# Kernel optimization log

Hardware: AMD Instinct MI355X
Metric: run time of the kernel (lower is better)

The kernel has to match this reference:

```python
import jax, jax.numpy as jnp
import numpy as np

N = 100_000        # nodes
F_IN = 1024        # input features
H1, C1 = 8, 8      # layer-1 heads, per-head channels (concat -> 64)
C_OUT = 40         # num classes (layer-2, heads=1, concat=False)
E = 3_200_000      # directed edges (avg degree 32)
NEG_SLOPE = 0.2    # PyG GATConv default leaky_relu slope


def setup_inputs() -> dict:
    key = jax.random.key(0)
    ks = jax.random.split(key, 10)
    x = jax.random.normal(ks[0], (N, F_IN), jnp.float32)
    edge_index = jax.random.randint(ks[1], (2, E), 0, N, dtype=jnp.int32)
    s1 = 1.0 / np.sqrt(F_IN)
    W1 = jax.random.normal(ks[2], (F_IN, H1 * C1), jnp.float32) * s1
    sa = 1.0 / np.sqrt(C1)
    att_src1 = jax.random.normal(ks[3], (H1, C1), jnp.float32) * sa
    att_dst1 = jax.random.normal(ks[4], (H1, C1), jnp.float32) * sa
    b1 = jnp.zeros((H1 * C1,), jnp.float32)
    s2 = 1.0 / np.sqrt(H1 * C1)
    W2 = jax.random.normal(ks[5], (H1 * C1, C_OUT), jnp.float32) * s2
    so = 1.0 / np.sqrt(C_OUT)
    att_src2 = jax.random.normal(ks[6], (1, C_OUT), jnp.float32) * so
    att_dst2 = jax.random.normal(ks[7], (1, C_OUT), jnp.float32) * so
    b2 = jnp.zeros((C_OUT,), jnp.float32)
    return {"x": x, "edge_index": edge_index, "W1": W1, "att_src1": att_src1,
            "att_dst1": att_dst1, "b1": b1, "W2": W2, "att_src2": att_src2,
            "att_dst2": att_dst2, "b2": b2}


def gat_layer(x, src, dst, W, a_src, a_dst, b, heads, ch, concat, n):
    # per-head linear projection: [n, heads, ch]
    xw = (x @ W).reshape(n, heads, ch)
    # per-node attention logits: [n, heads]
    al_src = jnp.einsum('nhc,hc->nh', xw, a_src)
    al_dst = jnp.einsum('nhc,hc->nh', xw, a_dst)
    # per-edge scores (message src -> dst): [e, heads]
    e = jax.nn.leaky_relu(al_src[src] + al_dst[dst], NEG_SLOPE)
    # segment softmax over incoming edges of each dst node
    m = jax.ops.segment_max(e, dst, num_segments=n)          # [n, heads]
    p = jnp.exp(e - m[dst])
    denom = jax.ops.segment_sum(p, dst, num_segments=n)      # [n, heads]
    alpha = p / (denom[dst] + 1e-16)                          # [e, heads]
    # weighted scatter-sum of source features
    out = jax.ops.segment_sum(xw[src] * alpha[:, :, None], dst, num_segments=n)
    out = out.reshape(n, heads * ch) if concat else out.mean(axis=1)
    return out + b


def reference(x, edge_index, W1, att_src1, att_dst1, b1, W2, att_src2, att_dst2, b2):
    n = x.shape[0]
    # PyG GATConv default: add self loops
    loop = jnp.arange(n, dtype=edge_index.dtype)
    src = jnp.concatenate([edge_index[0], loop])
    dst = jnp.concatenate([edge_index[1], loop])
    h = jax.nn.elu(gat_layer(x, src, dst, W1, att_src1, att_dst1, b1, H1, C1, True, n))
    h = gat_layer(h, src, dst, W2, att_src2, att_dst2, b2, 1, C_OUT, False, n)
    return jax.nn.log_softmax(h, axis=1)
```

## Files before the change

### kernel.cpp

```cpp
#include <hip/hip_runtime.h>
#include <hip/hip_bf16.h>
#include <cstdint>
#include <cstddef>

#define F_IN 1024
#define F1 64
#define H1 8
#define C1 8
#define C_OUT 40
#define XW2S 64
#define NEG 0.2f
#define LOG2E 1.442695040888963387f
#define B1 256
#define BSHIFT 8
#define BNODES 256

typedef __attribute__((ext_vector_type(8))) short short8;
typedef __attribute__((ext_vector_type(4))) float f32x4;

static __device__ __forceinline__ unsigned short f2bf(float f) {
  union { float f; unsigned u; } v; v.f = f;
  unsigned r = v.u + 0x7fff + ((v.u >> 16) & 1);
  return (unsigned short)(r >> 16);
}
static __device__ __forceinline__ float bf2f(unsigned short h) {
  union { unsigned u; float f; } v; v.u = ((unsigned)h) << 16; return v.f;
}
static __device__ __forceinline__ unsigned pkbf(float a, float b) {
  union { __hip_bfloat162 h; unsigned u; } c;
  c.h = __float22bfloat162_rn(float2{a, b});
  return c.u;
}
static __device__ __forceinline__ int rfl(int v) {
  return __builtin_amdgcn_readfirstlane(v);
}

__global__ __launch_bounds__(256) void w1cvt_kernel(const float* __restrict__ W1,
                                                    unsigned short* __restrict__ w1t) {
  int i = blockIdx.x * 256 + threadIdx.x;
  int c = i >> 10, k = i & 1023;
  w1t[i] = f2bf(W1[(size_t)k * F1 + c]);
}

__global__ __launch_bounds__(256) void k1_hist_gemm(const float* __restrict__ x,
    const unsigned short* __restrict__ w1t, unsigned short* __restrict__ xw1,
    const int* __restrict__ dst, int* __restrict__ cnt, int n, int e, int nbuck) {
  const int bid = blockIdx.x;
  const int tid = threadIdx.x;
  if (bid < B1) {
    __shared__ int lh[512];
    lh[tid] = 0; lh[tid + 256] = 0;
    __syncthreads();
    int chunk = (e + B1 - 1) / B1;
    int s = bid * chunk, en = min(e, s + chunk);
    for (int i = s + tid; i < en; i += 256) atomicAdd(&lh[dst[i] >> BSHIFT], 1);
    __syncthreads();
    for (int b = tid; b < nbuck; b += 256) cnt[b * B1 + bid] = lh[b];
    return;
  }
  const int gb = bid - B1;
  const int wv = tid >> 6;
  const int l = tid & 63;
  const int lr = l & 15;
  const int lg = l >> 4;
  const int rowBase = gb * 128 + wv * 32;
  int r0 = rowBase + lr, r1 = rowBase + 16 + lr;
  int r0c = r0 < n ? r0 : (n - 1);
  int r1c = r1 < n ? r1 : (n - 1);
  const float* px0 = x + (size_t)r0c * F_IN + lg * 8;
  const float* px1 = x + (size_t)r1c * F_IN + lg * 8;

  f32x4 acc00 = {0.f,0.f,0.f,0.f}, acc01 = acc00, acc02 = acc00, acc03 = acc00;
  f32x4 acc10 = acc00, acc11 = acc00, acc12 = acc00, acc13 = acc00;

#pragma unroll 2
  for (int k0 = 0; k0 < F_IN; k0 += 32) {
    float4 xa0 = *(const float4*)(px0 + k0);
    float4 xb0 = *(const float4*)(px0 + k0 + 4);
    float4 xa1 = *(const float4*)(px1 + k0);
    float4 xb1 = *(const float4*)(px1 + k0 + 4);
    union { short8 s; unsigned u[4]; } a0, a1;
    a0.u[0] = pkbf(xa0.x, xa0.y); a0.u[1] = pkbf(xa0.z, xa0.w);
    a0.u[2] = pkbf(xb0.x, xb0.y); a0.u[3] = pkbf(xb0.z, xb0.w);
    a1.u[0] = pkbf(xa1.x, xa1.y); a1.u[1] = pkbf(xa1.z, xa1.w);
    a1.u[2] = pkbf(xb1.x, xb1.y); a1.u[3] = pkbf(xb1.z, xb1.w);
    const size_t kOff = (size_t)(k0 + lg * 8);
    short8 b0 = *(const short8*)(w1t + (size_t)(0 * 16 + lr) * F_IN + kOff);
    short8 b1 = *(const short8*)(w1t + (size_t)(1 * 16 + lr) * F_IN + kOff);
    short8 b2 = *(const short8*)(w1t + (size_t)(2 * 16 + lr) * F_IN + kOff);
    short8 b3 = *(const short8*)(w1t + (size_t)(3 * 16 + lr) * F_IN + kOff);
    acc00 = __builtin_amdgcn_mfma_f32_16x16x32_bf16(a0.s, b0, acc00, 0, 0, 0);
    acc01 = __builtin_amdgcn_mfma_f32_16x16x32_bf16(a0.s, b1, acc01, 0, 0, 0);
    acc02 = __builtin_amdgcn_mfma_f32_16x16x32_bf16(a0.s, b2, acc02, 0, 0, 0);
    acc03 = __builtin_amdgcn_mfma_f32_16x16x32_bf16(a0.s, b3, acc03, 0, 0, 0);
    acc10 = __builtin_amdgcn_mfma_f32_16x16x32_bf16(a1.s, b0, acc10, 0, 0, 0);
    acc11 = __builtin_amdgcn_mfma_f32_16x16x32_bf16(a1.s, b1, acc11, 0, 0, 0);
    acc12 = __builtin_amdgcn_mfma_f32_16x16x32_bf16(a1.s, b2, acc12, 0, 0, 0);
    acc13 = __builtin_amdgcn_mfma_f32_16x16x32_bf16(a1.s, b3, acc13, 0, 0, 0);
  }

#pragma unroll
  for (int r = 0; r < 4; ++r) {
    int o0 = rowBase + lg * 4 + r;
    if (o0 < n) {
      unsigned short* po = xw1 + (size_t)o0 * F1 + lr;
      po[0]  = f2bf(acc00[r]);
      po[16] = f2bf(acc01[r]);
      po[32] = f2bf(acc02[r]);
      po[48] = f2bf(acc03[r]);
    }
    int o1 = rowBase + 16 + lg * 4 + r;
    if (o1 < n) {
      unsigned short* po = xw1 + (size_t)o1 * F1 + lr;
      po[0]  = f2bf(acc10[r]);
      po[16] = f2bf(acc11[r]);
      po[32] = f2bf(acc12[r]);
      po[48] = f2bf(acc13[r]);
    }
  }
}

__global__ __launch_bounds__(256) void al1_kernel(const unsigned short* __restrict__ xw1,
    const float* __restrict__ asrc, const float* __restrict__ adst,
    float* __restrict__ al_src, float* __restrict__ al_dst, int n) {
  int id = blockIdx.x * 256 + threadIdx.x;
  if (id >= n * H1) return;
  int node = id >> 3, h = id & 7;
  union { short8 s; unsigned short u[8]; } rowv;
  rowv.s = *(const short8*)(xw1 + (size_t)node * F1 + h * C1);
  float s = 0.f, d = 0.f;
#pragma unroll
  for (int c = 0; c < C1; ++c) {
    float v = bf2f(rowv.u[c]);
    s += v * asrc[h * C1 + c];
    d += v * adst[h * C1 + c];
  }
  al_src[id] = s * LOG2E;
  al_dst[id] = d * LOG2E;
}

__global__ __launch_bounds__(256) void scan1_kernel(const int* __restrict__ in,
    int* __restrict__ excl, int* __restrict__ bsum, int len) {
  __shared__ int s[256];
  int tid = threadIdx.x;
  int gid = blockIdx.x * 256 + tid;
  int v = gid < len ? in[gid] : 0;
  s[tid] = v;
  __syncthreads();
  for (int ofs = 1; ofs < 256; ofs <<= 1) {
    int t = (tid >= ofs) ? s[tid - ofs] : 0;
    __syncthreads();
    s[tid] += t;
    __syncthreads();
  }
  if (gid < len) excl[gid] = s[tid] - v;
  if (tid == 255) bsum[blockIdx.x] = s[255];
}

__global__ __launch_bounds__(1024) void scan2_kernel(int* __restrict__ bsum, int nb) {
  __shared__ int s[1024];
  int tid = threadIdx.x;
  int v = tid < nb ? bsum[tid] : 0;
  s[tid] = v;
  __syncthreads();
  for (int ofs = 1; ofs < 1024; ofs <<= 1) {
    int t = (tid >= ofs) ? s[tid - ofs] : 0;
    __syncthreads();
    s[tid] += t;
    __syncthreads();
  }
  if (tid < nb) bsum[tid] = s[tid] - v;
}

__global__ __launch_bounds__(256) void binscatter_kernel(const int* __restrict__ src,
    const int* __restrict__ dst, const int* __restrict__ cntS,
    const int* __restrict__ bsum, unsigned* __restrict__ binned, int e, int nbuck) {
  __shared__ int lcur[512];
  int tid = threadIdx.x, blk = blockIdx.x;
  for (int b = tid; b < nbuck; b += 256) lcur[b] = cntS[b * B1 + blk] + bsum[b];
  __syncthreads();
  int chunk = (e + gridDim.x - 1) / gridDim.x;
  int s = blk * chunk, en = min(e, s + chunk);
  for (int i = s + tid; i < en; i += 256) {
    int d = dst[i];
    int pos = atomicAdd(&lcur[d >> BSHIFT], 1);
    binned[pos] = ((unsigned)(d & (BNODES - 1)) << 23) | (unsigned)src[i];
  }
}

__global__ __launch_bounds__(256) void bucket_csr_kernel(const unsigned* __restrict__ binned,
    const int* __restrict__ bsum, int* __restrict__ deg, int* __restrict__ off,
    int* __restrict__ csr, int e, int n, int nbuck) {
  int q = blockIdx.x, tid = threadIdx.x;
  int eBase = bsum[q];
  int eEnd = (q + 1 < nbuck) ? bsum[q + 1] : e;
  __shared__ int nh[BNODES], sc[BNODES], cu[BNODES];
  nh[tid] = 0;
  __syncthreads();
  for (int i = eBase + tid; i < eEnd; i += 256) atomicAdd(&nh[binned[i] >> 23], 1);
  __syncthreads();
  int v = nh[tid];
  sc[tid] = v;
  __syncthreads();
  for (int ofs = 1; ofs < BNODES; ofs <<= 1) {
    int t = (tid >= ofs) ? sc[tid - ofs] : 0;
    __syncthreads();
    sc[tid] += t;
    __syncthreads();
  }
  int ex = sc[tid] - v;
  cu[tid] = ex;
  int node0 = q * BNODES + tid;
  if (node0 < n) { deg[node0] = v; off[node0] = eBase + ex; }
  __syncthreads();
  for (int i = eBase + tid; i < eEnd; i += 256) {
    unsigned w = binned[i];
    int pos = eBase + atomicAdd(&cu[w >> 23], 1);
    csr[pos] = (int)(w & 0x7FFFFF);
  }
}

__global__ __launch_bounds__(256) void gat1_agg(const unsigned short* __restrict__ xw1,
    const float* __restrict__ al_src, const float* __restrict__ al_dst,
    const int* __restrict__ csr, const int* __restrict__ off, const int* __restrict__ deg,
    const float* __restrict__ b1, float* __restrict__ h1, int n) {
  const int node = rfl((int)((blockIdx.x * blockDim.x + threadIdx.x) >> 6));
  if (node >= n) return;
  const int lane = threadIdx.x & 63;
  const int half = lane >> 5;
  const int c2 = lane & 31;
  const int h = c2 >> 2;
  const int base = rfl(off[node]);
  const int cnt = rfl(deg[node]);
  const float adst = al_dst[node * H1 + h];
  const int* __restrict__ csrp = csr + base;
  const char* xwB = (const char*)xw1;
  const char* alB = (const char*)al_src;
  const int cOff = c2 << 2;
  const int hOff = h << 2;

  float acc0 = 0.f, acc1 = 0.f, l = 0.f;

#define PAIR_BODY(wv_, av_) { \
    float t = (av_) + adst; \
    float sc = fmaxf(t, NEG * t); \
    float p = __builtin_amdgcn_exp2f(sc); \
    acc0 = fmaf(p, bf2f((unsigned short)((wv_) & 0xffffu)), acc0); \
    acc1 = fmaf(p, bf2f((unsigned short)((wv_) >> 16)), acc1); \
    l += p; }

  int it = 0;
  for (; it + 16 <= cnt; it += 16) {
    int xo[8];
#pragma unroll
    for (int jp = 0; jp < 8; ++jp) {
      int s0 = rfl(csrp[it + 2 * jp]) << 7;
      int s1 = rfl(csrp[it + 2 * jp + 1]) << 7;
      xo[jp] = half ? s1 : s0;
    }
    unsigned wv[8]; float av[8];
#pragma unroll
    for (int jp = 0; jp < 8; ++jp) {
      wv[jp] = *(const unsigned*)(xwB + xo[jp] + cOff);
      av[jp] = *(const float*)(alB + (xo[jp] >> 2) + hOff);
    }
#pragma unroll
    for (int jp = 0; jp < 8; ++jp) PAIR_BODY(wv[jp], av[jp]);
  }
  for (; it + 2 <= cnt; it += 2) {
    int s0 = rfl(csrp[it]) << 7;
    int s1 = rfl(csrp[it + 1]) << 7;
    int bs = half ? s1 : s0;
    unsigned w = *(const unsigned*)(xwB + bs + cOff);
    float av = *(const float*)(alB + (bs >> 2) + hOff);
    PAIR_BODY(w, av);
  }
  {
    const bool odd = (it < cnt);
    int sA = odd ? rfl(csrp[it]) : node;
    int bs = (half ? node : sA) << 7;
    unsigned w = *(const unsigned*)(xwB + bs + cOff);
    float av = *(const float*)(alB + (bs >> 2) + hOff);
    float t = av + adst;
    float sc = fmaxf(t, NEG * t);
    float p = __builtin_amdgcn_exp2f(sc);
    if (!odd && half) p = 0.f;
    acc0 = fmaf(p, bf2f((unsigned short)(w & 0xffffu)), acc0);
    acc1 = fmaf(p, bf2f((unsigned short)(w >> 16)), acc1);
    l += p;
  }
#undef PAIR_BODY

  acc0 += __shfl_xor(acc0, 32);
  acc1 += __shfl_xor(acc1, 32);
  l    += __shfl_xor(l, 32);
  if (half == 0) {
    float inv = 1.f / (l + 1e-16f);
    float2 bv = *(const float2*)(b1 + (c2 << 1));
    float o0 = acc0 * inv + bv.x;
    float o1 = acc1 * inv + bv.y;
    o0 = o0 > 0.f ? o0 : __expf(o0) - 1.f;
    o1 = o1 > 0.f ? o1 : __expf(o1) - 1.f;
    *(float2*)(h1 + (size_t)node * F1 + (c2 << 1)) = make_float2(o0, o1);
  }
}

__global__ __launch_bounds__(256) void gemm2_kernel(const float* __restrict__ h1,
    const float* __restrict__ W2, const float* __restrict__ asrc,
    const float* __restrict__ adst, unsigned short* __restrict__ xw2,
    float* __restrict__ alS2, float* __restrict__ alD2, int n) {
  __shared__ float ws[F1 * C_OUT];
  __shared__ float wsa[C_OUT], wsd[C_OUT];
  int tid = threadIdx.x;
  for (int i = tid; i < F1 * C_OUT; i += 256) ws[i] = W2[i];
  if (tid < C_OUT) { wsa[tid] = asrc[tid]; wsd[tid] = adst[tid]; }
  __syncthreads();
  int node = blockIdx.x * 256 + tid;
  if (node >= n) return;
  const float4* row4 = (const float4*)(h1 + (size_t)node * F1);
  float acc[C_OUT];
#pragma unroll
  for (int j = 0; j < C_OUT; ++j) acc[j] = 0.f;
#pragma unroll 2
  for (int k4 = 0; k4 < 16; ++k4) {
    float4 xv = row4[k4];
    const float* w0 = &ws[(4 * k4 + 0) * C_OUT];
    const float* w1 = &ws[(4 * k4 + 1) * C_OUT];
    const float* w2 = &ws[(4 * k4 + 2) * C_OUT];
    const float* w3 = &ws[(4 * k4 + 3) * C_OUT];
#pragma unroll
    for (int j = 0; j < C_OUT; j += 4) {
      float4 v0 = *(const float4*)(w0 + j);
      float4 v1 = *(const float4*)(w1 + j);
      float4 v2 = *(const float4*)(w2 + j);
      float4 v3 = *(const float4*)(w3 + j);
      acc[j + 0] += xv.x * v0.x + xv.y * v1.x + xv.z * v2.x + xv.w * v3.x;
      acc[j + 1] += xv.x * v0.y + xv.y * v1.y + xv.z * v2.y + xv.w * v3.y;
      acc[j + 2] += xv.x * v0.z + xv.y * v1.z + xv.z * v2.z + xv.w * v3.z;
      acc[j + 3] += xv.x * v0.w + xv.y * v1.w + xv.z * v2.w + xv.w * v3.w;
    }
  }
  float s = 0.f, d = 0.f;
#pragma unroll
  for (int j = 0; j < C_OUT; ++j) { s += acc[j] * wsa[j]; d += acc[j] * wsd[j]; }
  alS2[node] = s * LOG2E;
  alD2[node] = d * LOG2E;
  unsigned short* orow = xw2 + (size_t)node * XW2S;
#pragma unroll
  for (int j = 0; j < C_OUT; j += 4) {
    ushort4 o;
    o.x = f2bf(acc[j + 0]); o.y = f2bf(acc[j + 1]);
    o.z = f2bf(acc[j + 2]); o.w = f2bf(acc[j + 3]);
    *(ushort4*)(orow + j) = o;
  }
}

__global__ __launch_bounds__(256) void gat2_agg(const unsigned short* __restrict__ xw2,
    const float* __restrict__ alS, const float* __restrict__ alD,
    const int* __restrict__ csr, const int* __restrict__ off, const int* __restrict__ deg,
    const float* __restrict__ b2, float* __restrict__ out, int n) {
  const int node = rfl((int)((blockIdx.x * blockDim.x + threadIdx.x) >> 6));
  if (node >= n) return;
  const int lane = threadIdx.x & 63;
  const int half = lane >> 5;
  const int c2 = lane & 31;
  const bool act = c2 < 20;
  const int c2r = act ? c2 : 0;
  const int base = rfl(off[node]);
  const int cnt = rfl(deg[node]);
  const float adst = alD[node];
  const int* __restrict__ csrp = csr + base;
  const char* xwB = (const char*)xw2;
  const char* alB = (const char*)alS;
  const int cOff = c2r << 2;

  float acc0 = 0.f, acc1 = 0.f, l = 0.f;

#define PAIR_BODY2(wv_, av_) { \
    float t = (av_) + adst; \
    float sc = fmaxf(t, NEG * t); \
    float p = __builtin_amdgcn_exp2f(sc); \
    acc0 = fmaf(p, bf2f((unsigned short)((wv_) & 0xffffu)), acc0); \
    acc1 = fmaf(p, bf2f((unsigned short)((wv_) >> 16)), acc1); \
    l += p; }

  int it = 0;
  for (; it + 16 <= cnt; it += 16) {
    int xo[8];
#pragma unroll
    for (int jp = 0; jp < 8; ++jp) {
      int s0 = rfl(csrp[it + 2 * jp]) << 7;
      int s1 = rfl(csrp[it + 2 * jp + 1]) << 7;
      xo[jp] = half ? s1 : s0;
    }
    unsigned wv[8]; float av[8];
#pragma unroll
    for (int jp = 0; jp < 8; ++jp) {
      wv[jp] = *(const unsigned*)(xwB + xo[jp] + cOff);
      av[jp] = *(const float*)(alB + (xo[jp] >> 5));
    }
#pragma unroll
    for (int jp = 0; jp < 8; ++jp) PAIR_BODY2(wv[jp], av[jp]);
  }
  for (; it + 2 <= cnt; it += 2) {
    int s0 = rfl(csrp[it]) << 7;
    int s1 = rfl(csrp[it + 1]) << 7;
    int bs = half ? s1 : s0;
    unsigned w = *(const unsigned*)(xwB + bs + cOff);
    float av = *(const float*)(alB + (bs >> 5));
    PAIR_BODY2(w, av);
  }
  {
    const bool odd = (it < cnt);
    int sA = odd ? rfl(csrp[it]) : node;
    int bs = (half ? node : sA) << 7;
    unsigned w = *(const unsigned*)(xwB + bs + cOff);
    float av = *(const float*)(alB + (bs >> 5));
    float t = av + adst;
    float sc = fmaxf(t, NEG * t);
    float p = __builtin_amdgcn_exp2f(sc);
    if (!odd && half) p = 0.f;
    acc0 = fmaf(p, bf2f((unsigned short)(w & 0xffffu)), acc0);
    acc1 = fmaf(p, bf2f((unsigned short)(w >> 16)), acc1);
    l += p;
  }
#undef PAIR_BODY2

  acc0 += __shfl_xor(acc0, 32);
  acc1 += __shfl_xor(acc1, 32);
  l    += __shfl_xor(l, 32);

  float inv = 1.f / (l + 1e-16f);
  float v0 = -1e30f, v1 = -1e30f;
  if (act) {
    float2 bv = *(const float2*)(b2 + (c2 << 1));
    v0 = acc0 * inv + bv.x;
    v1 = acc1 * inv + bv.y;
  }
  float mx = fmaxf(v0, v1);
#pragma unroll
  for (int mask = 1; mask <= 16; mask <<= 1) mx = fmaxf(mx, __shfl_xor(mx, mask));
  float e0 = act ? __expf(v0 - mx) : 0.f;
  float e1 = act ? __expf(v1 - mx) : 0.f;
  float sum = e0 + e1;
#pragma unroll
  for (int mask = 1; mask <= 16; mask <<= 1) sum += __shfl_xor(sum, mask);
  if (half == 0 && act) {
    float ls = __logf(sum);
    *(float2*)(out + (size_t)node * C_OUT + (c2 << 1)) =
        make_float2(v0 - mx - ls, v1 - mx - ls);
  }
}

extern "C" void kernel_launch(void* const* d_in, const int* in_sizes, int n_in,
                              void* d_out, int out_size, void* d_ws, size_t ws_size,
                              hipStream_t stream) {
  const float* x   = (const float*)d_in[0];
  const int*   ei  = (const int*)d_in[1];
  const float* W1  = (const float*)d_in[2];
  const float* as1 = (const float*)d_in[3];
  const float* ad1 = (const float*)d_in[4];
  const float* b1  = (const float*)d_in[5];
  const float* W2  = (const float*)d_in[6];
  const float* as2 = (const float*)d_in[7];
  const float* ad2 = (const float*)d_in[8];
  const float* b2  = (const float*)d_in[9];
  float* out = (float*)d_out;

  const int n = in_sizes[0] / F_IN;
  const int e = in_sizes[1] / 2;
  const int* srcIdx = ei;
  const int* dstIdx = ei + e;
  const int nbuck = (n + BNODES - 1) >> BSHIFT;
  const int clen = nbuck * B1;

  char* p = (char*)d_ws;
  auto take = [&](size_t bytes) {
    char* q = p;
    p += (bytes + 255) & ~(size_t)255;
    return q;
  };
  unsigned short* xw1 = (unsigned short*)take((size_t)n * F1 * 2);
  float* h1           = (float*)take((size_t)n * F1 * 4);
  unsigned short* xw2 = (unsigned short*)take((size_t)n * XW2S * 2);
  unsigned short* w1t = (unsigned short*)take((size_t)F_IN * F1 * 2);
  float* alS1 = (float*)take((size_t)n * H1 * 4);
  float* alD1 = (float*)take((size_t)n * H1 * 4);
  float* alS2 = (float*)take((size_t)n * 4);
  float* alD2 = (float*)take((size_t)n * 4);
  int* deg  = (int*)take((size_t)n * 4);
  int* offb = (int*)take((size_t)n * 4);
  int* cnt  = (int*)take((size_t)clen * 4);
  int* cntS = (int*)take((size_t)clen * 4);
  int* bsum = (int*)take(4096);
  unsigned* binned = (unsigned*)take((size_t)e * 4);
  int* csr  = (int*)take((size_t)e * 4);

  dim3 b256(256);
  const int gB = (n + 127) / 128;
  w1cvt_kernel<<<dim3((F_IN * F1) / 256), b256, 0, stream>>>(W1, w1t);
  k1_hist_gemm<<<dim3(B1 + gB), b256, 0, stream>>>(x, w1t, xw1, dstIdx, cnt, n, e, nbuck);
  al1_kernel<<<dim3((n * H1 + 255) / 256), b256, 0, stream>>>(xw1, as1, ad1, alS1, alD1, n);

  int nbScan = (clen + 255) / 256;
  scan1_kernel<<<dim3(nbScan), b256, 0, stream>>>(cnt, cntS, bsum, clen);
  scan2_kernel<<<dim3(1), dim3(1024), 0, stream>>>(bsum, nbScan);
  binscatter_kernel<<<dim3(B1), b256, 0, stream>>>(srcIdx, dstIdx, cntS, bsum, binned, e, nbuck);
  bucket_csr_kernel<<<dim3(nbuck), b256, 0, stream>>>(binned, bsum, deg, offb, csr, e, n, nbuck);

  gat1_agg<<<dim3((n + 3) / 4), b256, 0, stream>>>(xw1, alS1, alD1, csr, offb, deg, b1, h1, n);
  gemm2_kernel<<<dim3((n + 255) / 256), b256, 0, stream>>>(h1, W2, as2, ad2, xw2, alS2, alD2, n);
  gat2_agg<<<dim3((n + 3) / 4), b256, 0, stream>>>(xw2, alS2, alD2, csr, offb, deg, b2, out, n);
}
```

Before: 408.7 us.

## Regroup preprocessing kernels to overlap graph binning with dense GEMM work

Reorders the launch sequence so the histogram is fused with W1 conversion, the bin-scatter is fused with the layer-1 GEMM, and the bucket CSR build is fused with the attention-logit kernel. Blocks of different roles in one launch run concurrently, so memory-bound scatter work overlaps the compute-bound GEMM. It also cuts the number of launches. The risk is that heterogeneous blocks compete for occupancy, and the GEMM now waits for the scans to finish.

Result: slower. 433.4 us (+6.0%).

```diff
diff --git a/kernel.cpp b/kernel.cpp
--- a/kernel.cpp
+++ b/kernel.cpp
@@ -35,16 +35,9 @@
   return __builtin_amdgcn_readfirstlane(v);
 }
 
-__global__ __launch_bounds__(256) void w1cvt_kernel(const float* __restrict__ W1,
-                                                    unsigned short* __restrict__ w1t) {
-  int i = blockIdx.x * 256 + threadIdx.x;
-  int c = i >> 10, k = i & 1023;
-  w1t[i] = f2bf(W1[(size_t)k * F1 + c]);
-}
-
-__global__ __launch_bounds__(256) void k1_hist_gemm(const float* __restrict__ x,
-    const unsigned short* __restrict__ w1t, unsigned short* __restrict__ xw1,
-    const int* __restrict__ dst, int* __restrict__ cnt, int n, int e, int nbuck) {
+__global__ __launch_bounds__(256) void k0_hist_w1cvt(const int* __restrict__ dst,
+    int* __restrict__ cnt, const float* __restrict__ W1,
+    unsigned short* __restrict__ w1t, int e, int nbuck) {
   const int bid = blockIdx.x;
   const int tid = threadIdx.x;
   if (bid < B1) {
@@ -56,6 +49,64 @@
     for (int i = s + tid; i < en; i += 256) atomicAdd(&lh[dst[i] >> BSHIFT], 1);
     __syncthreads();
     for (int b = tid; b < nbuck; b += 256) cnt[b * B1 + bid] = lh[b];
+    return;
+  }
+  int i = (bid - B1) * 256 + tid;
+  int c = i >> 10, k = i & 1023;
+  w1t[i] = f2bf(W1[(size_t)k * F1 + c]);
+}
+
+__global__ __launch_bounds__(256) void scan1_kernel(const int* __restrict__ in,
+    int* __restrict__ excl, int* __restrict__ bsum, int len) {
+  __shared__ int s[256];
+  int tid = threadIdx.x;
+  int gid = blockIdx.x * 256 + tid;
+  int v = gid < len ? in[gid] : 0;
+  s[tid] = v;
+  __syncthreads();
+  for (int ofs = 1; ofs < 256; ofs <<= 1) {
+    int t = (tid >= ofs) ? s[tid - ofs] : 0;
+    __syncthreads();
+    s[tid] += t;
+    __syncthreads();
+  }
+  if (gid < len) excl[gid] = s[tid] - v;
+  if (tid == 255) bsum[blockIdx.x] = s[255];
+}
+
+__global__ __launch_bounds__(1024) void scan2_kernel(int* __restrict__ bsum, int nb) {
+  __shared__ int s[1024];
+  int tid = threadIdx.x;
+  int v = tid < nb ? bsum[tid] : 0;
+  s[tid] = v;
+  __syncthreads();
+  for (int ofs = 1; ofs < 1024; ofs <<= 1) {
+    int t = (tid >= ofs) ? s[tid - ofs] : 0;
+    __syncthreads();
+    s[tid] += t;
+    __syncthreads();
+  }
+  if (tid < nb) bsum[tid] = s[tid] - v;
+}
+
+__global__ __launch_bounds__(256) void k3_scatter_gemm(const float* __restrict__ x,
+    const unsigned short* __restrict__ w1t, unsigned short* __restrict__ xw1,
+    const int* __restrict__ src, const int* __restrict__ dst,
+    const int* __restrict__ cntS, const int* __restrict__ bsum,
+    unsigned* __restrict__ binned, int n, int e, int nbuck) {
+  const int bid = blockIdx.x;
+  const int tid = threadIdx.x;
+  if (bid < B1) {
+    __shared__ int lcur[512];
+    for (int b = tid; b < nbuck; b += 256) lcur[b] = cntS[b * B1 + bid] + bsum[b];
+    __syncthreads();
+    int chunk = (e + B1 - 1) / B1;
+    int s = bid * chunk, en = min(e, s + chunk);
+    for (int i = s + tid; i < en; i += 256) {
+      int d = dst[i];
+      int pos = atomicAdd(&lcur[d >> BSHIFT], 1);
+      binned[pos] = ((unsigned)(d & (BNODES - 1)) << 23) | (unsigned)src[i];
+    }
     return;
   }
   const int gb = bid - B1;
@@ -120,10 +171,44 @@
   }
 }
 
-__global__ __launch_bounds__(256) void al1_kernel(const unsigned short* __restrict__ xw1,
+__global__ __launch_bounds__(256) void k4_bucket_al1(const unsigned* __restrict__ binned,
+    const int* __restrict__ bsum, int* __restrict__ deg, int* __restrict__ off,
+    int* __restrict__ csr, const unsigned short* __restrict__ xw1,
     const float* __restrict__ asrc, const float* __restrict__ adst,
-    float* __restrict__ al_src, float* __restrict__ al_dst, int n) {
-  int id = blockIdx.x * 256 + threadIdx.x;
+    float* __restrict__ al_src, float* __restrict__ al_dst, int e, int n, int nbuck) {
+  const int bid = blockIdx.x;
+  const int tid = threadIdx.x;
+  if (bid < nbuck) {
+    int q = bid;
+    int eBase = bsum[q];
+    int eEnd = (q + 1 < nbuck) ? bsum[q + 1] : e;
+    __shared__ int nh[BNODES], sc[BNODES], cu[BNODES];
+    nh[tid] = 0;
+    __syncthreads();
+    for (int i = eBase + tid; i < eEnd; i += 256) atomicAdd(&nh[binned[i] >> 23], 1);
+    __syncthreads();
+    int v = nh[tid];
+    sc[tid] = v;
+    __syncthreads();
+    for (int ofs = 1; ofs < BNODES; ofs <<= 1) {
+      int t = (tid >= ofs) ? sc[tid - ofs] : 0;
+      __syncthreads();
+      sc[tid] += t;
+      __syncthreads();
+    }
+    int ex = sc[tid] - v;
+    cu[tid] = ex;
+    int node0 = q * BNODES + tid;
+    if (node0 < n) { deg[node0] = v; off[node0] = eBase + ex; }
+    __syncthreads();
+    for (int i = eBase + tid; i < eEnd; i += 256) {
+      unsigned w = binned[i];
+      int pos = eBase + atomicAdd(&cu[w >> 23], 1);
+      csr[pos] = (int)(w & 0x7FFFFF);
+    }
+    return;
+  }
+  int id = (bid - nbuck) * 256 + tid;
   if (id >= n * H1) return;
   int node = id >> 3, h = id & 7;
   union { short8 s; unsigned short u[8]; } rowv;
@@ -137,87 +222,6 @@
   }
   al_src[id] = s * LOG2E;
   al_dst[id] = d * LOG2E;
-}
-
-__global__ __launch_bounds__(256) void scan1_kernel(const int* __restrict__ in,
-    int* __restrict__ excl, int* __restrict__ bsum, int len) {
-  __shared__ int s[256];
-  int tid = threadIdx.x;
-  int gid = blockIdx.x * 256 + tid;
-  int v = gid < len ? in[gid] : 0;
-  s[tid] = v;
-  __syncthreads();
-  for (int ofs = 1; ofs < 256; ofs <<= 1) {
-    int t = (tid >= ofs) ? s[tid - ofs] : 0;
-    __syncthreads();
-    s[tid] += t;
-    __syncthreads();
-  }
-  if (gid < len) excl[gid] = s[tid] - v;
-  if (tid == 255) bsum[blockIdx.x] = s[255];
-}
-
-__global__ __launch_bounds__(1024) void scan2_kernel(int* __restrict__ bsum, int nb) {
-  __shared__ int s[1024];
-  int tid = threadIdx.x;
-  int v = tid < nb ? bsum[tid] : 0;
-  s[tid] = v;
-  __syncthreads();
-  for (int ofs = 1; ofs < 1024; ofs <<= 1) {
-    int t = (tid >= ofs) ? s[tid - ofs] : 0;
-    __syncthreads();
-    s[tid] += t;
-    __syncthreads();
-  }
-  if (tid < nb) bsum[tid] = s[tid] - v;
-}
-
-__global__ __launch_bounds__(256) void binscatter_kernel(const int* __restrict__ src,
-    const int* __restrict__ dst, const int* __restrict__ cntS,
-    const int* __restrict__ bsum, unsigned* __restrict__ binned, int e, int nbuck) {
-  __shared__ int lcur[512];
-  int tid = threadIdx.x, blk = blockIdx.x;
-  for (int b = tid; b < nbuck; b += 256) lcur[b] = cntS[b * B1 + blk] + bsum[b];
-  __syncthreads();
-  int chunk = (e + gridDim.x - 1) / gridDim.x;
-  int s = blk * chunk, en = min(e, s + chunk);
-  for (int i = s + tid; i < en; i += 256) {
-    int d = dst[i];
-    int pos = atomicAdd(&lcur[d >> BSHIFT], 1);
-    binned[pos] = ((unsigned)(d & (BNODES - 1)) << 23) | (unsigned)src[i];
-  }
-}
-
-__global__ __launch_bounds__(256) void bucket_csr_kernel(const unsigned* __restrict__ binned,
-    const int* __restrict__ bsum, int* __restrict__ deg, int* __restrict__ off,
-    int* __restrict__ csr, int e, int n, int nbuck) {
-  int q = blockIdx.x, tid = threadIdx.x;
-  int eBase = bsum[q];
-  int eEnd = (q + 1 < nbuck) ? bsum[q + 1] : e;
-  __shared__ int nh[BNODES], sc[BNODES], cu[BNODES];
-  nh[tid] = 0;
-  __syncthreads();
-  for (int i = eBase + tid; i < eEnd; i += 256) atomicAdd(&nh[binned[i] >> 23], 1);
-  __syncthreads();
-  int v = nh[tid];
-  sc[tid] = v;
-  __syncthreads();
-  for (int ofs = 1; ofs < BNODES; ofs <<= 1) {
-    int t = (tid >= ofs) ? sc[tid - ofs] : 0;
-    __syncthreads();
-    sc[tid] += t;
-    __syncthreads();
-  }
-  int ex = sc[tid] - v;
-  cu[tid] = ex;
-  int node0 = q * BNODES + tid;
-  if (node0 < n) { deg[node0] = v; off[node0] = eBase + ex; }
-  __syncthreads();
-  for (int i = eBase + tid; i < eEnd; i += 256) {
-    unsigned w = binned[i];
-    int pos = eBase + atomicAdd(&cu[w >> 23], 1);
-    csr[pos] = (int)(w & 0x7FFFFF);
-  }
 }
 
 __global__ __launch_bounds__(256) void gat1_agg(const unsigned short* __restrict__ xw1,
@@ -498,15 +502,17 @@
 
   dim3 b256(256);
   const int gB = (n + 127) / 128;
-  w1cvt_kernel<<<dim3((F_IN * F1) / 256), b256, 0, stream>>>(W1, w1t);
-  k1_hist_gemm<<<dim3(B1 + gB), b256, 0, stream>>>(x, w1t, xw1, dstIdx, cnt, n, e, nbuck);
-  al1_kernel<<<dim3((n * H1 + 255) / 256), b256, 0, stream>>>(xw1, as1, ad1, alS1, alD1, n);
-
+  const int alBlocks = (n * H1 + 255) / 256;
+  const int w1Blocks = (F_IN * F1) / 256;
   int nbScan = (clen + 255) / 256;
+
+  k0_hist_w1cvt<<<dim3(B1 + w1Blocks), b256, 0, stream>>>(dstIdx, cnt, W1, w1t, e, nbuck);
   scan1_kernel<<<dim3(nbScan), b256, 0, stream>>>(cnt, cntS, bsum, clen);
   scan2_kernel<<<dim3(1), dim3(1024), 0, stream>>>(bsum, nbScan);
-  binscatter_kernel<<<dim3(B1), b256, 0, stream>>>(srcIdx, dstIdx, cntS, bsum, binned, e, nbuck);
-  bucket_csr_kernel<<<dim3(nbuck), b256, 0, stream>>>(binned, bsum, deg, offb, csr, e, n, nbuck);
+  k3_scatter_gemm<<<dim3(B1 + gB), b256, 0, stream>>>(x, w1t, xw1, srcIdx, dstIdx,
+      cntS, bsum, binned, n, e, nbuck);
+  k4_bucket_al1<<<dim3(nbuck + alBlocks), b256, 0, stream>>>(binned, bsum, deg, offb,
+      csr, xw1, as1, ad1, alS1, alD1, e, n, nbuck);
 
   gat1_agg<<<dim3((n + 3) / 4), b256, 0, stream>>>(xw1, alS1, alD1, csr, offb, deg, b1, h1, n);
   gemm2_kernel<<<dim3((n + 255) / 256), b256, 0, stream>>>(h1, W2, as2, ad2, xw2, alS2, alD2, n);
```
